# Kernel tuning notes

Measured on AMD Instinct MI355X. Metric: run time of the kernel, lower is better.

The kernel has to match this reference:

```python
import jax, jax.numpy as jnp
import numpy as np

D_MODEL = 1024
N_HEAD = 16
D_K = D_MODEL // N_HEAD
SCALE = float(np.sqrt(D_K))


def setup_inputs() -> dict:
    key = jax.random.key(0)
    ks = jax.random.split(key, 11)
    B, S = 2, 2048
    inp = {
        "q": jax.random.normal(ks[0], (B, S, D_MODEL), dtype=jnp.float32),
        "k": jax.random.normal(ks[1], (B, S, D_MODEL), dtype=jnp.float32),
        "v": jax.random.normal(ks[2], (B, S, D_MODEL), dtype=jnp.float32),
    }
    std = 1.0 / np.sqrt(D_MODEL)
    for i, name in enumerate(["Wq", "Wk", "Wv", "Wo"]):
        inp[name] = jax.random.normal(ks[3 + i], (D_MODEL, D_MODEL), dtype=jnp.float32) * std
        inp["b" + name[1:]] = jax.random.normal(ks[7 + i], (D_MODEL,), dtype=jnp.float32) * 0.01
    return inp


def reference(q, k, v, Wq, bq, Wk, bk, Wv, bv, Wo, bo):
    B, S, _ = q.shape
    # QKV projections -> [B, H, S, Dk]
    def split_heads(x):
        return x.reshape(B, -1, N_HEAD, D_K).transpose(0, 2, 1, 3)

    qh = split_heads(q @ Wq + bq)
    kh = split_heads(k @ Wk + bk)
    vh = split_heads(v @ Wv + bv)
    # scaled dot-product attention (full score matrix, as in the torch module)
    scores = jnp.einsum("bhqd,bhkd->bhqk", qh, kh) / SCALE
    attn_weights = jax.nn.softmax(scores, axis=-1)
    ctx = jnp.einsum("bhqk,bhkd->bhqd", attn_weights, vh)
    ctx = ctx.transpose(0, 2, 1, 3).reshape(B, S, D_MODEL)
    output = ctx @ Wo + bo
    return (output, attn_weights)
```

## Files before the change

kernel.cpp:

```cpp
#include <hip/hip_runtime.h>

#define NB 2
#define NH 16
#define SS 2048
#define DM 1024
#define DK 64
#define MM 4096

typedef __attribute__((ext_vector_type(8))) short short8;
typedef __attribute__((ext_vector_type(4))) float floatx4;
typedef unsigned short u16;
typedef unsigned int u32;

#define WS_X    0
#define WS_WT   25165824
#define WS_QH   33554432
#define WS_KH   41943040
#define WS_VH   50331648
#define WS_VT   58720256
#define WS_CTX  67108864

__device__ inline u16 f2bf(float f) {
    union { float f; u32 u; } x; x.f = f;
    u32 u = x.u;
    return (u16)((u + 0x7fffu + ((u >> 16) & 1u)) >> 16);
}

__global__ __launch_bounds__(256) void wcast_kernel(
    const float* __restrict__ Wq, const float* __restrict__ Wk,
    const float* __restrict__ Wv, const float* __restrict__ Wo,
    u16* __restrict__ wt)
{
    __shared__ float tile[32][33];
    int mat = blockIdx.z;
    const float* W = (mat == 0) ? Wq : (mat == 1) ? Wk : (mat == 2) ? Wv : Wo;
    u16* Wt = wt + (size_t)mat * (DM * DM);
    int bx = blockIdx.x * 32, by = blockIdx.y * 32;
    int tx = threadIdx.x & 31, ty = threadIdx.x >> 5;
#pragma unroll
    for (int k = 0; k < 4; k++)
        tile[ty + k * 8][tx] = W[(by + ty + k * 8) * DM + bx + tx];
    __syncthreads();
#pragma unroll
    for (int k = 0; k < 4; k++)
        Wt[(bx + ty + k * 8) * DM + by + tx] = f2bf(tile[tx][ty + k * 8]);
}

__global__ __launch_bounds__(256) void xcast_kernel(
    const float* __restrict__ q, const float* __restrict__ k,
    const float* __restrict__ v, u16* __restrict__ x)
{
    int seg = blockIdx.y;
    const float* src = (seg == 0) ? q : (seg == 1) ? k : v;
    u16* dst = x + (size_t)seg * (MM * DM);
    int i = blockIdx.x * 256 + threadIdx.x;
    float4 f = ((const float4*)src)[i];
    u32 lo = (u32)f2bf(f.x) | ((u32)f2bf(f.y) << 16);
    u32 hi = (u32)f2bf(f.z) | ((u32)f2bf(f.w) << 16);
    ((uint2*)dst)[i] = make_uint2(lo, hi);
}

__global__ __launch_bounds__(256) void proj_kernel(
    const u16* __restrict__ X, const u16* __restrict__ WT,
    const float* __restrict__ bq, const float* __restrict__ bk,
    const float* __restrict__ bv,
    u16* __restrict__ qh, u16* __restrict__ kh, u16* __restrict__ vh)
{
    int mode = blockIdx.z;
    const u16* A  = X  + (size_t)mode * (MM * DM);
    const u16* Bt = WT + (size_t)mode * (DM * DM);
    const float* bias = (mode == 0) ? bq : (mode == 1) ? bk : bv;
    u16* out = (mode == 0) ? qh : (mode == 1) ? kh : vh;

    __shared__ u16 As[64][40];
    __shared__ u16 Bs[64][40];

    int m0 = blockIdx.y * 64, n0 = blockIdx.x * 64;
    int t = threadIdx.x, wave = t >> 6, lane = t & 63;
    int quad = lane >> 4, c = lane & 15;
    int wm = wave >> 1, wn = wave & 1;
    int ar = t >> 2, ac = (t & 3) * 8;

    floatx4 acc[2][2];
#pragma unroll
    for (int i = 0; i < 2; i++)
#pragma unroll
        for (int j = 0; j < 2; j++)
            acc[i][j] = (floatx4){0.f, 0.f, 0.f, 0.f};

    for (int k0 = 0; k0 < DM; k0 += 32) {
        *(uint4*)&As[ar][ac] = *(const uint4*)&A[(size_t)(m0 + ar) * DM + k0 + ac];
        *(uint4*)&Bs[ar][ac] = *(const uint4*)&Bt[(size_t)(n0 + ar) * DM + k0 + ac];
        __syncthreads();
        short8 af[2], bf[2];
        af[0] = *(short8*)&As[wm * 32 + c][quad * 8];
        af[1] = *(short8*)&As[wm * 32 + 16 + c][quad * 8];
        bf[0] = *(short8*)&Bs[wn * 32 + c][quad * 8];
        bf[1] = *(short8*)&Bs[wn * 32 + 16 + c][quad * 8];
#pragma unroll
        for (int mi = 0; mi < 2; mi++)
#pragma unroll
            for (int ni = 0; ni < 2; ni++)
                acc[mi][ni] = __builtin_amdgcn_mfma_f32_16x16x32_bf16(
                    af[mi], bf[ni], acc[mi][ni], 0, 0, 0);
        __syncthreads();
    }

#pragma unroll
    for (int mi = 0; mi < 2; mi++)
#pragma unroll
        for (int ni = 0; ni < 2; ni++) {
            int col = n0 + wn * 32 + ni * 16 + c;
            float bs = bias[col];
            int h = col >> 6, dk = col & 63;
#pragma unroll
            for (int r = 0; r < 4; r++) {
                int row = m0 + wm * 32 + mi * 16 + quad * 4 + r;
                float v = acc[mi][ni][r] + bs;
                if (mode == 0) v *= 0.125f;
                int b = row >> 11, s = row & 2047;
                out[(((size_t)(b * NH + h)) * SS + s) * DK + dk] = f2bf(v);
            }
        }
}

__global__ __launch_bounds__(256) void vtrans_kernel(
    const u16* __restrict__ vh, u16* __restrict__ vt)
{
    __shared__ u16 tile[32][33];
    int bh = blockIdx.z;
    const u16* src = vh + (size_t)bh * SS * DK;
    u16* dst = vt + (size_t)bh * DK * SS;
    int bx = blockIdx.x * 32;
    int by = blockIdx.y * 32;
    int tx = threadIdx.x & 31, ty = threadIdx.x >> 5;
#pragma unroll
    for (int k = 0; k < 4; k++)
        tile[ty + k * 8][tx] = src[(size_t)(by + ty + k * 8) * DK + bx + tx];
    __syncthreads();
#pragma unroll
    for (int k = 0; k < 4; k++)
        dst[(size_t)(bx + ty + k * 8) * SS + by + tx] = tile[tx][ty + k * 8];
}

__global__ __launch_bounds__(256) void attn_kernel(
    const u16* __restrict__ qh, const u16* __restrict__ kh,
    const u16* __restrict__ vt, u16* __restrict__ ctx,
    float* __restrict__ attw)
{
    int bh = blockIdx.y;
    int q0 = blockIdx.x * 64;
    const u16* Q  = qh + (size_t)bh * SS * DK;
    const u16* K  = kh + (size_t)bh * SS * DK;
    const u16* Vt = vt + (size_t)bh * DK * SS;

    int t = threadIdx.x, w = t >> 6, lane = t & 63;
    int quad = lane >> 4, c = lane & 15;

    __shared__ u16 Ks[32][72];
    __shared__ u16 Vs[64][40];
    __shared__ u16 Ps[4][16][40];

    const u16* qrow = Q + (size_t)(q0 + w * 16 + c) * DK;
    short8 aq[2];
    aq[0] = *(const short8*)(qrow + quad * 8);
    aq[1] = *(const short8*)(qrow + 32 + quad * 8);

    float m_r[4], l_r[4];
    floatx4 cacc[4];
#pragma unroll
    for (int r = 0; r < 4; r++) { m_r[r] = -1e30f; l_r[r] = 0.f; }
#pragma unroll
    for (int dt = 0; dt < 4; dt++) cacc[dt] = (floatx4){0.f, 0.f, 0.f, 0.f};

    int kr = t >> 3, ko = (t & 7) * 8;
    int vr = t >> 2, vo = (t & 3) * 8;

    for (int kt = 0; kt < SS; kt += 32) {
        *(uint4*)&Ks[kr][ko] = *(const uint4*)&K[(size_t)(kt + kr) * DK + ko];
        *(uint4*)&Vs[vr][vo] = *(const uint4*)&Vt[(size_t)vr * SS + kt + vo];
        __syncthreads();

        floatx4 sacc[2];
        sacc[0] = (floatx4){0.f, 0.f, 0.f, 0.f};
        sacc[1] = (floatx4){0.f, 0.f, 0.f, 0.f};
#pragma unroll
        for (int nt = 0; nt < 2; nt++)
#pragma unroll
            for (int kk = 0; kk < 2; kk++) {
                short8 bk_ = *(short8*)&Ks[nt * 16 + c][kk * 32 + quad * 8];
                sacc[nt] = __builtin_amdgcn_mfma_f32_16x16x32_bf16(
                    aq[kk], bk_, sacc[nt], 0, 0, 0);
            }

        float p0[4], p1[4];
#pragma unroll
        for (int r = 0; r < 4; r++) {
            float mx = fmaxf(sacc[0][r], sacc[1][r]);
#pragma unroll
            for (int off = 8; off; off >>= 1)
                mx = fmaxf(mx, __shfl_xor(mx, off));
            float mnew = fmaxf(m_r[r], mx);
            float alpha = __expf(m_r[r] - mnew);
            m_r[r] = mnew;
            float s0 = __expf(sacc[0][r] - mnew);
            float s1 = __expf(sacc[1][r] - mnew);
            p0[r] = s0; p1[r] = s1;
            float rs = s0 + s1;
#pragma unroll
            for (int off = 8; off; off >>= 1)
                rs += __shfl_xor(rs, off);
            l_r[r] = l_r[r] * alpha + rs;
#pragma unroll
            for (int dt = 0; dt < 4; dt++) cacc[dt][r] *= alpha;
        }

#pragma unroll
        for (int r = 0; r < 4; r++) {
            Ps[w][quad * 4 + r][c]      = f2bf(p0[r]);
            Ps[w][quad * 4 + r][16 + c] = f2bf(p1[r]);
        }
        short8 ap = *(short8*)&Ps[w][c][quad * 8];
#pragma unroll
        for (int dt = 0; dt < 4; dt++) {
            short8 bv_ = *(short8*)&Vs[dt * 16 + c][quad * 8];
            cacc[dt] = __builtin_amdgcn_mfma_f32_16x16x32_bf16(
                ap, bv_, cacc[dt], 0, 0, 0);
        }
        __syncthreads();
    }

    int b = bh >> 4, h = bh & 15;
#pragma unroll
    for (int r = 0; r < 4; r++) {
        float rl = 1.0f / l_r[r];
        int qrow_g = q0 + w * 16 + quad * 4 + r;
        size_t orow = (size_t)(b * SS + qrow_g) * DM + h * DK;
#pragma unroll
        for (int dt = 0; dt < 4; dt++)
            ctx[orow + dt * 16 + c] = f2bf(cacc[dt][r] * rl);
    }

    float rl_r[4];
#pragma unroll
    for (int r = 0; r < 4; r++) rl_r[r] = 1.0f / l_r[r];

    float* awb = attw + (size_t)bh * ((size_t)SS * SS);
    for (int kt = 0; kt < SS; kt += 32) {
        *(uint4*)&Ks[kr][ko] = *(const uint4*)&K[(size_t)(kt + kr) * DK + ko];
        __syncthreads();
        floatx4 sacc[2];
        sacc[0] = (floatx4){0.f, 0.f, 0.f, 0.f};
        sacc[1] = (floatx4){0.f, 0.f, 0.f, 0.f};
#pragma unroll
        for (int nt = 0; nt < 2; nt++)
#pragma unroll
            for (int kk = 0; kk < 2; kk++) {
                short8 bk_ = *(short8*)&Ks[nt * 16 + c][kk * 32 + quad * 8];
                sacc[nt] = __builtin_amdgcn_mfma_f32_16x16x32_bf16(
                    aq[kk], bk_, sacc[nt], 0, 0, 0);
            }
#pragma unroll
        for (int nt = 0; nt < 2; nt++)
#pragma unroll
            for (int r = 0; r < 4; r++) {
                int row = q0 + w * 16 + quad * 4 + r;
                float wgt = __expf(sacc[nt][r] - m_r[r]) * rl_r[r];
                awb[(size_t)row * SS + kt + nt * 16 + c] = wgt;
            }
        __syncthreads();
    }
}

__global__ __launch_bounds__(256) void outproj_kernel(
    const u16* __restrict__ A, const u16* __restrict__ Bt,
    const float* __restrict__ bias, float* __restrict__ out)
{
    __shared__ u16 As[64][40];
    __shared__ u16 Bs[64][40];
    int m0 = blockIdx.y * 64, n0 = blockIdx.x * 64;
    int t = threadIdx.x, wave = t >> 6, lane = t & 63;
    int quad = lane >> 4, c = lane & 15;
    int wm = wave >> 1, wn = wave & 1;
    int ar = t >> 2, ac = (t & 3) * 8;

    floatx4 acc[2][2];
#pragma unroll
    for (int i = 0; i < 2; i++)
#pragma unroll
        for (int j = 0; j < 2; j++)
            acc[i][j] = (floatx4){0.f, 0.f, 0.f, 0.f};

    for (int k0 = 0; k0 < DM; k0 += 32) {
        *(uint4*)&As[ar][ac] = *(const uint4*)&A[(size_t)(m0 + ar) * DM + k0 + ac];
        *(uint4*)&Bs[ar][ac] = *(const uint4*)&Bt[(size_t)(n0 + ar) * DM + k0 + ac];
        __syncthreads();
        short8 af[2], bf[2];
        af[0] = *(short8*)&As[wm * 32 + c][quad * 8];
        af[1] = *(short8*)&As[wm * 32 + 16 + c][quad * 8];
        bf[0] = *(short8*)&Bs[wn * 32 + c][quad * 8];
        bf[1] = *(short8*)&Bs[wn * 32 + 16 + c][quad * 8];
#pragma unroll
        for (int mi = 0; mi < 2; mi++)
#pragma unroll
            for (int ni = 0; ni < 2; ni++)
                acc[mi][ni] = __builtin_amdgcn_mfma_f32_16x16x32_bf16(
                    af[mi], bf[ni], acc[mi][ni], 0, 0, 0);
        __syncthreads();
    }

#pragma unroll
    for (int mi = 0; mi < 2; mi++)
#pragma unroll
        for (int ni = 0; ni < 2; ni++) {
            int col = n0 + wn * 32 + ni * 16 + c;
            float bs = bias[col];
#pragma unroll
            for (int r = 0; r < 4; r++) {
                int row = m0 + wm * 32 + mi * 16 + quad * 4 + r;
                out[(size_t)row * DM + col] = acc[mi][ni][r] + bs;
            }
        }
}

extern "C" void kernel_launch(void* const* d_in, const int* in_sizes, int n_in,
                              void* d_out, int out_size, void* d_ws, size_t ws_size,
                              hipStream_t stream)
{
    const float* q  = (const float*)d_in[0];
    const float* k  = (const float*)d_in[1];
    const float* v  = (const float*)d_in[2];
    const float* Wq = (const float*)d_in[3];
    const float* bq = (const float*)d_in[4];
    const float* Wk = (const float*)d_in[5];
    const float* bk = (const float*)d_in[6];
    const float* Wv = (const float*)d_in[7];
    const float* bv = (const float*)d_in[8];
    const float* Wo = (const float*)d_in[9];
    const float* bo = (const float*)d_in[10];
    float* out = (float*)d_out;
    char* ws = (char*)d_ws;

    u16* xq  = (u16*)(ws + WS_X);
    u16* wt  = (u16*)(ws + WS_WT);
    u16* qh  = (u16*)(ws + WS_QH);
    u16* kh  = (u16*)(ws + WS_KH);
    u16* vh  = (u16*)(ws + WS_VH);
    u16* vt  = (u16*)(ws + WS_VT);
    u16* ctx = (u16*)(ws + WS_CTX);

    wcast_kernel<<<dim3(32, 32, 4), 256, 0, stream>>>(Wq, Wk, Wv, Wo, wt);
    xcast_kernel<<<dim3(4096, 3), 256, 0, stream>>>(q, k, v, xq);
    proj_kernel<<<dim3(16, 64, 3), 256, 0, stream>>>(xq, wt, bq, bk, bv, qh, kh, vh);
    vtrans_kernel<<<dim3(2, 64, 32), 256, 0, stream>>>(vh, vt);
    attn_kernel<<<dim3(32, 32), 256, 0, stream>>>(qh, kh, vt, ctx, out + 4194304);
    outproj_kernel<<<dim3(16, 64), 256, 0, stream>>>(ctx, wt + 3 * (DM * DM), bo, out);
}
```

Before: 888.5 us.

## Restructure attention into stats pass plus fused weight-write/PV pass; enlarge GEMM tiles

The attention kernel now runs a first pass over K that computes only row max and sum, then a second pass that computes the normalized weights, stores them with nontemporal stores, and feeds the same weights into the P·V MFMAs. This replaces the earlier online-softmax PV loop followed by a separate weight-writing pass, and removes the per-tile rescaling of the accumulator. Key tiles grow to 64 and each wave handles 32 query rows, so each K/V tile is reused across more queries. The projection and output GEMMs move to 128-row tiles with 4x4 and 4x2 MFMA accumulator blocks, which raises register use and halves the number of blocks.

Result: faster. 860.0 us (-3.2%).

```diff
diff --git a/kernel.cpp b/kernel.cpp
--- a/kernel.cpp
+++ b/kernel.cpp
@@ -72,50 +72,54 @@
     const float* bias = (mode == 0) ? bq : (mode == 1) ? bk : bv;
     u16* out = (mode == 0) ? qh : (mode == 1) ? kh : vh;
 
-    __shared__ u16 As[64][40];
-    __shared__ u16 Bs[64][40];
-
-    int m0 = blockIdx.y * 64, n0 = blockIdx.x * 64;
+    __shared__ u16 As[128][40];
+    __shared__ u16 Bs[128][40];
+
+    int m0 = blockIdx.y * 128, n0 = blockIdx.x * 128;
     int t = threadIdx.x, wave = t >> 6, lane = t & 63;
     int quad = lane >> 4, c = lane & 15;
     int wm = wave >> 1, wn = wave & 1;
-    int ar = t >> 2, ac = (t & 3) * 8;
-
-    floatx4 acc[2][2];
-#pragma unroll
-    for (int i = 0; i < 2; i++)
-#pragma unroll
-        for (int j = 0; j < 2; j++)
+    int sr = t >> 2, sc4 = (t & 3) * 8;
+
+    floatx4 acc[4][4];
+#pragma unroll
+    for (int i = 0; i < 4; i++)
+#pragma unroll
+        for (int j = 0; j < 4; j++)
             acc[i][j] = (floatx4){0.f, 0.f, 0.f, 0.f};
 
     for (int k0 = 0; k0 < DM; k0 += 32) {
-        *(uint4*)&As[ar][ac] = *(const uint4*)&A[(size_t)(m0 + ar) * DM + k0 + ac];
-        *(uint4*)&Bs[ar][ac] = *(const uint4*)&Bt[(size_t)(n0 + ar) * DM + k0 + ac];
-        __syncthreads();
-        short8 af[2], bf[2];
-        af[0] = *(short8*)&As[wm * 32 + c][quad * 8];
-        af[1] = *(short8*)&As[wm * 32 + 16 + c][quad * 8];
-        bf[0] = *(short8*)&Bs[wn * 32 + c][quad * 8];
-        bf[1] = *(short8*)&Bs[wn * 32 + 16 + c][quad * 8];
-#pragma unroll
-        for (int mi = 0; mi < 2; mi++)
-#pragma unroll
-            for (int ni = 0; ni < 2; ni++)
+        *(uint4*)&As[sr][sc4]      = *(const uint4*)&A [(size_t)(m0 + sr) * DM + k0 + sc4];
+        *(uint4*)&As[sr + 64][sc4] = *(const uint4*)&A [(size_t)(m0 + sr + 64) * DM + k0 + sc4];
+        *(uint4*)&Bs[sr][sc4]      = *(const uint4*)&Bt[(size_t)(n0 + sr) * DM + k0 + sc4];
+        *(uint4*)&Bs[sr + 64][sc4] = *(const uint4*)&Bt[(size_t)(n0 + sr + 64) * DM + k0 + sc4];
+        __syncthreads();
+        short8 af[4], bf[4];
+#pragma unroll
+        for (int mi = 0; mi < 4; mi++)
+            af[mi] = *(short8*)&As[wm * 64 + mi * 16 + c][quad * 8];
+#pragma unroll
+        for (int ni = 0; ni < 4; ni++)
+            bf[ni] = *(short8*)&Bs[wn * 64 + ni * 16 + c][quad * 8];
+#pragma unroll
+        for (int mi = 0; mi < 4; mi++)
+#pragma unroll
+            for (int ni = 0; ni < 4; ni++)
                 acc[mi][ni] = __builtin_amdgcn_mfma_f32_16x16x32_bf16(
                     af[mi], bf[ni], acc[mi][ni], 0, 0, 0);
         __syncthreads();
     }
 
 #pragma unroll
-    for (int mi = 0; mi < 2; mi++)
-#pragma unroll
-        for (int ni = 0; ni < 2; ni++) {
-            int col = n0 + wn * 32 + ni * 16 + c;
+    for (int mi = 0; mi < 4; mi++)
+#pragma unroll
+        for (int ni = 0; ni < 4; ni++) {
+            int col = n0 + wn * 64 + ni * 16 + c;
             float bs = bias[col];
             int h = col >> 6, dk = col & 63;
 #pragma unroll
             for (int r = 0; r < 4; r++) {
-                int row = m0 + wm * 32 + mi * 16 + quad * 4 + r;
+                int row = m0 + wm * 64 + mi * 16 + quad * 4 + r;
                 float v = acc[mi][ni][r] + bs;
                 if (mode == 0) v *= 0.125f;
                 int b = row >> 11, s = row & 2047;
@@ -149,7 +153,7 @@
     float* __restrict__ attw)
 {
     int bh = blockIdx.y;
-    int q0 = blockIdx.x * 64;
+    int q0 = blockIdx.x * 128;
     const u16* Q  = qh + (size_t)bh * SS * DK;
     const u16* K  = kh + (size_t)bh * SS * DK;
     const u16* Vt = vt + (size_t)bh * DK * SS;
@@ -157,151 +161,187 @@
     int t = threadIdx.x, w = t >> 6, lane = t & 63;
     int quad = lane >> 4, c = lane & 15;
 
-    __shared__ u16 Ks[32][72];
-    __shared__ u16 Vs[64][40];
-    __shared__ u16 Ps[4][16][40];
-
-    const u16* qrow = Q + (size_t)(q0 + w * 16 + c) * DK;
-    short8 aq[2];
-    aq[0] = *(const short8*)(qrow + quad * 8);
-    aq[1] = *(const short8*)(qrow + 32 + quad * 8);
-
-    float m_r[4], l_r[4];
-    floatx4 cacc[4];
-#pragma unroll
-    for (int r = 0; r < 4; r++) { m_r[r] = -1e30f; l_r[r] = 0.f; }
-#pragma unroll
-    for (int dt = 0; dt < 4; dt++) cacc[dt] = (floatx4){0.f, 0.f, 0.f, 0.f};
-
-    int kr = t >> 3, ko = (t & 7) * 8;
-    int vr = t >> 2, vo = (t & 3) * 8;
-
-    for (int kt = 0; kt < SS; kt += 32) {
-        *(uint4*)&Ks[kr][ko] = *(const uint4*)&K[(size_t)(kt + kr) * DK + ko];
-        *(uint4*)&Vs[vr][vo] = *(const uint4*)&Vt[(size_t)vr * SS + kt + vo];
-        __syncthreads();
-
-        floatx4 sacc[2];
-        sacc[0] = (floatx4){0.f, 0.f, 0.f, 0.f};
-        sacc[1] = (floatx4){0.f, 0.f, 0.f, 0.f};
-#pragma unroll
-        for (int nt = 0; nt < 2; nt++)
-#pragma unroll
-            for (int kk = 0; kk < 2; kk++) {
-                short8 bk_ = *(short8*)&Ks[nt * 16 + c][kk * 32 + quad * 8];
-                sacc[nt] = __builtin_amdgcn_mfma_f32_16x16x32_bf16(
-                    aq[kk], bk_, sacc[nt], 0, 0, 0);
-            }
-
-        float p0[4], p1[4];
+    __shared__ u16 Ks[64][72];
+    __shared__ u16 Vs[64][72];
+    __shared__ u16 Ps[4][32][72];
+
+    int sr0 = t >> 3, sco = (t & 7) * 8;
+    int sr1 = sr0 + 32;
+
+    short8 aq[2][2];
+#pragma unroll
+    for (int m = 0; m < 2; m++) {
+        const u16* qr = Q + (size_t)(q0 + w * 32 + m * 16 + c) * DK;
+        aq[m][0] = *(const short8*)(qr + quad * 8);
+        aq[m][1] = *(const short8*)(qr + 32 + quad * 8);
+    }
+
+    float m_r[2][4], l_r[2][4];
+#pragma unroll
+    for (int m = 0; m < 2; m++)
+#pragma unroll
+        for (int r = 0; r < 4; r++) { m_r[m][r] = -1e30f; l_r[m][r] = 0.f; }
+
+    for (int kt = 0; kt < SS; kt += 64) {
+        *(uint4*)&Ks[sr0][sco] = *(const uint4*)&K[(size_t)(kt + sr0) * DK + sco];
+        *(uint4*)&Ks[sr1][sco] = *(const uint4*)&K[(size_t)(kt + sr1) * DK + sco];
+        __syncthreads();
+
+        floatx4 sacc[2][4];
+#pragma unroll
+        for (int m = 0; m < 2; m++)
+#pragma unroll
+            for (int nt = 0; nt < 4; nt++)
+                sacc[m][nt] = (floatx4){0.f, 0.f, 0.f, 0.f};
+#pragma unroll
+        for (int nt = 0; nt < 4; nt++) {
+            short8 b0 = *(short8*)&Ks[nt * 16 + c][quad * 8];
+            short8 b1 = *(short8*)&Ks[nt * 16 + c][32 + quad * 8];
+#pragma unroll
+            for (int m = 0; m < 2; m++) {
+                sacc[m][nt] = __builtin_amdgcn_mfma_f32_16x16x32_bf16(aq[m][0], b0, sacc[m][nt], 0, 0, 0);
+                sacc[m][nt] = __builtin_amdgcn_mfma_f32_16x16x32_bf16(aq[m][1], b1, sacc[m][nt], 0, 0, 0);
+            }
+        }
+
+#pragma unroll
+        for (int m = 0; m < 2; m++)
+#pragma unroll
+            for (int r = 0; r < 4; r++) {
+                float mx = fmaxf(fmaxf(sacc[m][0][r], sacc[m][1][r]),
+                                 fmaxf(sacc[m][2][r], sacc[m][3][r]));
+#pragma unroll
+                for (int off = 8; off; off >>= 1)
+                    mx = fmaxf(mx, __shfl_xor(mx, off));
+                float mo = m_r[m][r];
+                float mn = fmaxf(mo, mx);
+                float rs = __expf(sacc[m][0][r] - mn) + __expf(sacc[m][1][r] - mn)
+                         + __expf(sacc[m][2][r] - mn) + __expf(sacc[m][3][r] - mn);
+#pragma unroll
+                for (int off = 8; off; off >>= 1)
+                    rs += __shfl_xor(rs, off);
+                m_r[m][r] = mn;
+                l_r[m][r] = l_r[m][r] * __expf(mo - mn) + rs;
+            }
+        __syncthreads();
+    }
+
+    float rl[2][4];
+#pragma unroll
+    for (int m = 0; m < 2; m++)
+#pragma unroll
+        for (int r = 0; r < 4; r++) rl[m][r] = 1.0f / l_r[m][r];
+
+    floatx4 cacc[2][4];
+#pragma unroll
+    for (int m = 0; m < 2; m++)
+#pragma unroll
+        for (int dt = 0; dt < 4; dt++) cacc[m][dt] = (floatx4){0.f, 0.f, 0.f, 0.f};
+
+    float* awb = attw + (size_t)bh * ((size_t)SS * SS);
+
+    for (int kt = 0; kt < SS; kt += 64) {
+        *(uint4*)&Ks[sr0][sco] = *(const uint4*)&K[(size_t)(kt + sr0) * DK + sco];
+        *(uint4*)&Ks[sr1][sco] = *(const uint4*)&K[(size_t)(kt + sr1) * DK + sco];
+        *(uint4*)&Vs[sr0][sco] = *(const uint4*)&Vt[(size_t)sr0 * SS + kt + sco];
+        *(uint4*)&Vs[sr1][sco] = *(const uint4*)&Vt[(size_t)sr1 * SS + kt + sco];
+        __syncthreads();
+
+        floatx4 sacc[2][4];
+#pragma unroll
+        for (int m = 0; m < 2; m++)
+#pragma unroll
+            for (int nt = 0; nt < 4; nt++)
+                sacc[m][nt] = (floatx4){0.f, 0.f, 0.f, 0.f};
+#pragma unroll
+        for (int nt = 0; nt < 4; nt++) {
+            short8 b0 = *(short8*)&Ks[nt * 16 + c][quad * 8];
+            short8 b1 = *(short8*)&Ks[nt * 16 + c][32 + quad * 8];
+#pragma unroll
+            for (int m = 0; m < 2; m++) {
+                sacc[m][nt] = __builtin_amdgcn_mfma_f32_16x16x32_bf16(aq[m][0], b0, sacc[m][nt], 0, 0, 0);
+                sacc[m][nt] = __builtin_amdgcn_mfma_f32_16x16x32_bf16(aq[m][1], b1, sacc[m][nt], 0, 0, 0);
+            }
+        }
+
+#pragma unroll
+        for (int m = 0; m < 2; m++)
+#pragma unroll
+            for (int r = 0; r < 4; r++) {
+                size_t ro = (size_t)(q0 + w * 32 + m * 16 + quad * 4 + r) * SS + kt;
+                float mm = m_r[m][r], rr = rl[m][r];
+#pragma unroll
+                for (int nt = 0; nt < 4; nt++) {
+                    float wgt = __expf(sacc[m][nt][r] - mm) * rr;
+                    __builtin_nontemporal_store(wgt, &awb[ro + nt * 16 + c]);
+                    Ps[w][m * 16 + quad * 4 + r][nt * 16 + c] = f2bf(wgt);
+                }
+            }
+
+        short8 bv[4][2];
+#pragma unroll
+        for (int dt = 0; dt < 4; dt++) {
+            bv[dt][0] = *(short8*)&Vs[dt * 16 + c][quad * 8];
+            bv[dt][1] = *(short8*)&Vs[dt * 16 + c][32 + quad * 8];
+        }
+#pragma unroll
+        for (int m = 0; m < 2; m++) {
+            short8 ap0 = *(short8*)&Ps[w][m * 16 + c][quad * 8];
+            short8 ap1 = *(short8*)&Ps[w][m * 16 + c][32 + quad * 8];
+#pragma unroll
+            for (int dt = 0; dt < 4; dt++) {
+                cacc[m][dt] = __builtin_amdgcn_mfma_f32_16x16x32_bf16(ap0, bv[dt][0], cacc[m][dt], 0, 0, 0);
+                cacc[m][dt] = __builtin_amdgcn_mfma_f32_16x16x32_bf16(ap1, bv[dt][1], cacc[m][dt], 0, 0, 0);
+            }
+        }
+        __syncthreads();
+    }
+
+    int b = bh >> 4, h = bh & 15;
+#pragma unroll
+    for (int m = 0; m < 2; m++)
 #pragma unroll
         for (int r = 0; r < 4; r++) {
-            float mx = fmaxf(sacc[0][r], sacc[1][r]);
-#pragma unroll
-            for (int off = 8; off; off >>= 1)
-                mx = fmaxf(mx, __shfl_xor(mx, off));
-            float mnew = fmaxf(m_r[r], mx);
-            float alpha = __expf(m_r[r] - mnew);
-            m_r[r] = mnew;
-            float s0 = __expf(sacc[0][r] - mnew);
-            float s1 = __expf(sacc[1][r] - mnew);
-            p0[r] = s0; p1[r] = s1;
-            float rs = s0 + s1;
-#pragma unroll
-            for (int off = 8; off; off >>= 1)
-                rs += __shfl_xor(rs, off);
-            l_r[r] = l_r[r] * alpha + rs;
-#pragma unroll
-            for (int dt = 0; dt < 4; dt++) cacc[dt][r] *= alpha;
-        }
-
-#pragma unroll
-        for (int r = 0; r < 4; r++) {
-            Ps[w][quad * 4 + r][c]      = f2bf(p0[r]);
-            Ps[w][quad * 4 + r][16 + c] = f2bf(p1[r]);
-        }
-        short8 ap = *(short8*)&Ps[w][c][quad * 8];
-#pragma unroll
-        for (int dt = 0; dt < 4; dt++) {
-            short8 bv_ = *(short8*)&Vs[dt * 16 + c][quad * 8];
-            cacc[dt] = __builtin_amdgcn_mfma_f32_16x16x32_bf16(
-                ap, bv_, cacc[dt], 0, 0, 0);
-        }
-        __syncthreads();
-    }
-
-    int b = bh >> 4, h = bh & 15;
-#pragma unroll
-    for (int r = 0; r < 4; r++) {
-        float rl = 1.0f / l_r[r];
-        int qrow_g = q0 + w * 16 + quad * 4 + r;
-        size_t orow = (size_t)(b * SS + qrow_g) * DM + h * DK;
-#pragma unroll
-        for (int dt = 0; dt < 4; dt++)
-            ctx[orow + dt * 16 + c] = f2bf(cacc[dt][r] * rl);
-    }
-
-    float rl_r[4];
-#pragma unroll
-    for (int r = 0; r < 4; r++) rl_r[r] = 1.0f / l_r[r];
-
-    float* awb = attw + (size_t)bh * ((size_t)SS * SS);
-    for (int kt = 0; kt < SS; kt += 32) {
-        *(uint4*)&Ks[kr][ko] = *(const uint4*)&K[(size_t)(kt + kr) * DK + ko];
-        __syncthreads();
-        floatx4 sacc[2];
-        sacc[0] = (floatx4){0.f, 0.f, 0.f, 0.f};
-        sacc[1] = (floatx4){0.f, 0.f, 0.f, 0.f};
-#pragma unroll
-        for (int nt = 0; nt < 2; nt++)
-#pragma unroll
-            for (int kk = 0; kk < 2; kk++) {
-                short8 bk_ = *(short8*)&Ks[nt * 16 + c][kk * 32 + quad * 8];
-                sacc[nt] = __builtin_amdgcn_mfma_f32_16x16x32_bf16(
-                    aq[kk], bk_, sacc[nt], 0, 0, 0);
-            }
-#pragma unroll
-        for (int nt = 0; nt < 2; nt++)
-#pragma unroll
-            for (int r = 0; r < 4; r++) {
-                int row = q0 + w * 16 + quad * 4 + r;
-                float wgt = __expf(sacc[nt][r] - m_r[r]) * rl_r[r];
-                awb[(size_t)row * SS + kt + nt * 16 + c] = wgt;
-            }
-        __syncthreads();
-    }
+            size_t orow = (size_t)(b * SS + q0 + w * 32 + m * 16 + quad * 4 + r) * DM + h * DK;
+#pragma unroll
+            for (int dt = 0; dt < 4; dt++)
+                ctx[orow + dt * 16 + c] = f2bf(cacc[m][dt][r]);
+        }
 }
 
 __global__ __launch_bounds__(256) void outproj_kernel(
     const u16* __restrict__ A, const u16* __restrict__ Bt,
     const float* __restrict__ bias, float* __restrict__ out)
 {
-    __shared__ u16 As[64][40];
+    __shared__ u16 As[128][40];
     __shared__ u16 Bs[64][40];
-    int m0 = blockIdx.y * 64, n0 = blockIdx.x * 64;
+    int m0 = blockIdx.y * 128, n0 = blockIdx.x * 64;
     int t = threadIdx.x, wave = t >> 6, lane = t & 63;
     int quad = lane >> 4, c = lane & 15;
     int wm = wave >> 1, wn = wave & 1;
-    int ar = t >> 2, ac = (t & 3) * 8;
-
-    floatx4 acc[2][2];
-#pragma unroll
-    for (int i = 0; i < 2; i++)
+    int sr = t >> 2, sc4 = (t & 3) * 8;
+
+    floatx4 acc[4][2];
+#pragma unroll
+    for (int i = 0; i < 4; i++)
 #pragma unroll
         for (int j = 0; j < 2; j++)
             acc[i][j] = (floatx4){0.f, 0.f, 0.f, 0.f};
 
     for (int k0 = 0; k0 < DM; k0 += 32) {
-        *(uint4*)&As[ar][ac] = *(const uint4*)&A[(size_t)(m0 + ar) * DM + k0 + ac];
-        *(uint4*)&Bs[ar][ac] = *(const uint4*)&Bt[(size_t)(n0 + ar) * DM + k0 + ac];
-        __syncthreads();
-        short8 af[2], bf[2];
-        af[0] = *(short8*)&As[wm * 32 + c][quad * 8];
-        af[1] = *(short8*)&As[wm * 32 + 16 + c][quad * 8];
-        bf[0] = *(short8*)&Bs[wn * 32 + c][quad * 8];
-        bf[1] = *(short8*)&Bs[wn * 32 + 16 + c][quad * 8];
-#pragma unroll
-        for (int mi = 0; mi < 2; mi++)
+        *(uint4*)&As[sr][sc4]      = *(const uint4*)&A [(size_t)(m0 + sr) * DM + k0 + sc4];
+        *(uint4*)&As[sr + 64][sc4] = *(const uint4*)&A [(size_t)(m0 + sr + 64) * DM + k0 + sc4];
+        *(uint4*)&Bs[sr][sc4]      = *(const uint4*)&Bt[(size_t)(n0 + sr) * DM + k0 + sc4];
+        __syncthreads();
+        short8 af[4], bf[2];
+#pragma unroll
+        for (int mi = 0; mi < 4; mi++)
+            af[mi] = *(short8*)&As[wm * 64 + mi * 16 + c][quad * 8];
+#pragma unroll
+        for (int ni = 0; ni < 2; ni++)
+            bf[ni] = *(short8*)&Bs[wn * 32 + ni * 16 + c][quad * 8];
+#pragma unroll
+        for (int mi = 0; mi < 4; mi++)
 #pragma unroll
             for (int ni = 0; ni < 2; ni++)
                 acc[mi][ni] = __builtin_amdgcn_mfma_f32_16x16x32_bf16(
@@ -310,14 +350,14 @@
     }
 
 #pragma unroll
-    for (int mi = 0; mi < 2; mi++)
+    for (int mi = 0; mi < 4; mi++)
 #pragma unroll
         for (int ni = 0; ni < 2; ni++) {
             int col = n0 + wn * 32 + ni * 16 + c;
             float bs = bias[col];
 #pragma unroll
             for (int r = 0; r < 4; r++) {
-                int row = m0 + wm * 32 + mi * 16 + quad * 4 + r;
+                int row = m0 + wm * 64 + mi * 16 + quad * 4 + r;
                 out[(size_t)row * DM + col] = acc[mi][ni][r] + bs;
             }
         }
@@ -351,8 +391,8 @@
 
     wcast_kernel<<<dim3(32, 32, 4), 256, 0, stream>>>(Wq, Wk, Wv, Wo, wt);
     xcast_kernel<<<dim3(4096, 3), 256, 0, stream>>>(q, k, v, xq);
-    proj_kernel<<<dim3(16, 64, 3), 256, 0, stream>>>(xq, wt, bq, bk, bv, qh, kh, vh);
+    proj_kernel<<<dim3(8, 32, 3), 256, 0, stream>>>(xq, wt, bq, bk, bv, qh, kh, vh);
     vtrans_kernel<<<dim3(2, 64, 32), 256, 0, stream>>>(vh, vt);
-    attn_kernel<<<dim3(32, 32), 256, 0, stream>>>(qh, kh, vt, ctx, out + 4194304);
-    outproj_kernel<<<dim3(16, 64), 256, 0, stream>>>(ctx, wt + 3 * (DM * DM), bo, out);
-}
+    attn_kernel<<<dim3(16, 32), 256, 0, stream>>>(qh, kh, vt, ctx, out + 4194304);
+    outproj_kernel<<<dim3(16, 32), 256, 0, stream>>>(ctx, wt + 3 * (DM * DM), bo, out);
+}
```
